# Kernel tuning notes

Hardware: AMD Instinct MI355X
Metric: run time of the kernel (lower is better)

Reference implementation:

```python
import jax, jax.numpy as jnp
import numpy as np

B, D, V = 1024, 512, 100000
M = 0.4
EPS = 1e-07


def setup_inputs() -> dict:
    key = jax.random.key(0)
    k1, k2, k3 = jax.random.split(key, 3)
    inp = jax.random.normal(k1, (B, D), dtype=jnp.float32)
    # xavier_uniform for (D, V): limit = sqrt(6/(D+V))
    limit = float(np.sqrt(6.0 / (D + V)))
    weight = jax.random.uniform(k2, (D, V), dtype=jnp.float32, minval=-limit, maxval=limit)
    labels = jax.random.randint(k3, (B,), 0, V, dtype=jnp.int64)
    return {"input": inp, "weight": weight, "labels": labels}


def reference(input, weight, labels):
    # L2-normalize rows of input and columns of weight (F.normalize eps=1e-12)
    x_norm = input / jnp.maximum(jnp.linalg.norm(input, axis=1, keepdims=True), 1e-12)
    w_norm = weight / jnp.maximum(jnp.linalg.norm(weight, axis=0, keepdims=True), 1e-12)
    cosine = x_norm @ w_norm                                # [B, V]
    cosine = jnp.clip(cosine, -1.0 + EPS, 1.0 - EPS)
    arcos = jnp.arccos(cosine)
    # add margin m only at the label class (one-hot add without dense one-hot)
    rows = jnp.arange(B)
    arcos = arcos.at[rows, labels].add(M)
    logits = jnp.cos(arcos)                                 # [B, V]
    # cross-entropy, mean reduction
    logz = jax.nn.logsumexp(logits, axis=1)                 # [B]
    label_logit = logits[rows, labels]                      # [B]
    loss = jnp.mean(logz - label_logit)
    return loss
```

## Files before the change

### kernel.cpp

```cpp
#include <hip/hip_runtime.h>
#include <hip/hip_bf16.h>
#include <math.h>

#define B_    1024
#define D_    512
#define V_    100000
#define V_PAD 100096
#define NT_   782
#define EPS_  1e-7f
#define COSM  0.9210609940028851f
#define SINM  0.3894183423086505f

typedef __bf16 bf16x8 __attribute__((ext_vector_type(8)));
typedef float  f32x4  __attribute__((ext_vector_type(4)));

struct alignas(16) US8 { unsigned short h[8]; };

__device__ __forceinline__ unsigned short f2bf(float f) {
  union { float f; unsigned u; } a; a.f = f;
  unsigned u = a.u;
  u += 0x7FFFu + ((u >> 16) & 1u);
  return (unsigned short)(u >> 16);
}

__device__ __forceinline__ void async_copy16(void* lds, const void* g) {
  __builtin_amdgcn_global_load_lds(
      (const __attribute__((address_space(1))) void*)g,
      (__attribute__((address_space(3))) void*)lds, 16, 0, 0);
}

__global__ void x_prep(const float* __restrict__ x,
                       unsigned short* __restrict__ xb,
                       float* __restrict__ S) {
  int t = threadIdx.x;
  int lane = t & 63, wave = t >> 6;
  int row = blockIdx.x * 4 + wave;
  const float* xr = x + (size_t)row * D_;
  f32x4 a = *(const f32x4*)(xr + lane * 8);
  f32x4 b = *(const f32x4*)(xr + lane * 8 + 4);
  float ss = a[0]*a[0] + a[1]*a[1] + a[2]*a[2] + a[3]*a[3]
           + b[0]*b[0] + b[1]*b[1] + b[2]*b[2] + b[3]*b[3];
#pragma unroll
  for (int off = 32; off > 0; off >>= 1) ss += __shfl_xor(ss, off, 64);
  float inv = 1.0f / fmaxf(sqrtf(ss), 1e-12f);
  US8 pk;
#pragma unroll
  for (int j = 0; j < 4; ++j) pk.h[j]     = f2bf(a[j] * inv);
#pragma unroll
  for (int j = 0; j < 4; ++j) pk.h[4 + j] = f2bf(b[j] * inv);
  *(US8*)(xb + (size_t)row * D_ + lane * 8) = pk;
  if (lane == 0) S[row] = 0.0f;
}

__global__ __launch_bounds__(256) void w_cast2(const float* __restrict__ w,
                                               unsigned short* __restrict__ wbT,
                                               float* __restrict__ invw) {
  __shared__ unsigned short tile[64 * 512];
  __shared__ float red[4][64];
  int t = threadIdx.x;
  int c = t & 63;
  int wv = t >> 6;
  int vb = blockIdx.x * 64;
  bool valid = (vb + c) < V_;
  const float* wp = w + vb + c;
  float ss = 0.0f;
#pragma unroll
  for (int k = 0; k < 16; ++k) {
    int d0 = k * 32 + wv * 8;
    float v[8];
#pragma unroll
    for (int i = 0; i < 8; ++i)
      v[i] = valid ? wp[(size_t)(d0 + i) * V_] : 0.0f;
    US8 pk;
#pragma unroll
    for (int i = 0; i < 8; ++i) { ss += v[i] * v[i]; pk.h[i] = f2bf(v[i]); }
    int chunk = ((d0 >> 3) ^ c) & 63;
    *(US8*)&tile[c * 512 + chunk * 8] = pk;
  }
  red[wv][c] = ss;
  __syncthreads();
  if (t < 64) {
    float tot = red[0][t] + red[1][t] + red[2][t] + red[3][t];
    invw[vb + t] = ((vb + t) < V_) ? 1.0f / fmaxf(sqrtf(tot), 1e-12f) : 0.0f;
  }
#pragma unroll
  for (int i = 0; i < 16; ++i) {
    int cc = wv * 16 + i;
    US8 val = *(const US8*)&tile[cc * 512 + ((c ^ cc) & 63) * 8];
    *(US8*)(wbT + (size_t)(vb + cc) * D_ + c * 8) = val;
  }
}

#define BM 128
#define BN 128
#define BK 64

__global__ __launch_bounds__(256) void gemm_epi(
    const unsigned short* __restrict__ xb,
    const unsigned short* __restrict__ wbT,
    const float* __restrict__ invw,
    const int* __restrict__ labels,
    float* __restrict__ S, float* __restrict__ Lb) {
  int bid = blockIdx.x;
  int xcd = bid & 7;
  int slot = bid >> 3;
  int tn = xcd * 98 + (slot >> 3);
  int tm = slot & 7;
  if (tn >= NT_) return;
  int m0 = tm * BM, n0 = tn * BN;

  __shared__ unsigned short Ab[BM * BK];
  __shared__ unsigned short Bb[BN * BK];
  __shared__ int labT[BM];
  int t = threadIdx.x;
  if (t < BM) labT[t] = labels[m0 + t];
  int lane = t & 63;
  int q = lane >> 4, l15 = lane & 15;
  int wave = t >> 6;
  int wm = (wave & 1) * 64, wn = (wave >> 1) * 64;
  f32x4 acc[4][4] = {};

  const unsigned short* gA[4];
  const unsigned short* gB[4];
#pragma unroll
  for (int j = 0; j < 4; ++j) {
    int p = t + 256 * j;
    int m = p >> 3;
    int kc = (p & 7) ^ (m & 7);
    gA[j] = xb  + (size_t)(m0 + m) * D_ + kc * 8;
    gB[j] = wbT + (size_t)(n0 + m) * D_ + kc * 8;
  }

  for (int kt = 0; kt < D_; kt += BK) {
#pragma unroll
    for (int j = 0; j < 4; ++j) {
      async_copy16(Ab + (t + 256 * j) * 8, gA[j] + kt);
      async_copy16(Bb + (t + 256 * j) * 8, gB[j] + kt);
    }
    __syncthreads();
    int h = l15 & 7;
#pragma unroll
    for (int s = 0; s < 2; ++s) {
      int kx = s * 4 + q;
      bf16x8 af[4], bfr[4];
#pragma unroll
      for (int ri = 0; ri < 4; ++ri) {
        int row = wm + ri * 16 + l15;
        af[ri] = *(const bf16x8*)&Ab[(row * 8 + (kx ^ h)) * 8];
      }
#pragma unroll
      for (int ci = 0; ci < 4; ++ci) {
        int row = wn + ci * 16 + l15;
        bfr[ci] = *(const bf16x8*)&Bb[(row * 8 + (kx ^ h)) * 8];
      }
#pragma unroll
      for (int ri = 0; ri < 4; ++ri)
#pragma unroll
        for (int ci = 0; ci < 4; ++ci)
          acc[ri][ci] = __builtin_amdgcn_mfma_f32_16x16x32_bf16(
              af[ri], bfr[ci], acc[ri][ci], 0, 0, 0);
    }
    __syncthreads();
  }

  float iw[4]; int vcol[4];
#pragma unroll
  for (int ci = 0; ci < 4; ++ci) {
    vcol[ci] = n0 + wn + ci * 16 + l15;
    iw[ci] = invw[vcol[ci]];
  }
#pragma unroll
  for (int ri = 0; ri < 4; ++ri) {
#pragma unroll
    for (int reg = 0; reg < 4; ++reg) {
      int ml = wm + ri * 16 + q * 4 + reg;
      int r = m0 + ml;
      int lab = labT[ml];
      float s = 0.0f;
#pragma unroll
      for (int ci = 0; ci < 4; ++ci) {
        float cv = acc[ri][ci][reg] * iw[ci];
        cv = fminf(fmaxf(cv, -1.0f + EPS_), 1.0f - EPS_);
        float logit = cv;
        if (vcol[ci] == lab) {
          logit = cv * COSM - sqrtf(fmaxf(1.0f - cv * cv, 0.0f)) * SINM;
          Lb[r] = logit;
        }
        s += (vcol[ci] < V_) ? __expf(logit) : 0.0f;
      }
      s += __shfl_xor(s, 1, 64);
      s += __shfl_xor(s, 2, 64);
      s += __shfl_xor(s, 4, 64);
      s += __shfl_xor(s, 8, 64);
      if (l15 == 0) atomicAdd(&S[r], s);
    }
  }
}

__global__ void finalk(const float* __restrict__ S, const float* __restrict__ Lb,
                       float* __restrict__ out) {
  __shared__ float red[256];
  int t = threadIdx.x;
  float s = 0.0f;
  for (int i = t; i < B_; i += 256) s += logf(S[i]) - Lb[i];
  red[t] = s;
  __syncthreads();
  for (int o = 128; o > 0; o >>= 1) {
    if (t < o) red[t] += red[t + o];
    __syncthreads();
  }
  if (t == 0) out[0] = red[0] * (1.0f / B_);
}

extern "C" void kernel_launch(void* const* d_in, const int* in_sizes, int n_in,
                              void* d_out, int out_size, void* d_ws, size_t ws_size,
                              hipStream_t stream) {
  const float* x = (const float*)d_in[0];
  const float* w = (const float*)d_in[1];
  const int* labels = (const int*)d_in[2];
  float* out = (float*)d_out;
  char* ws = (char*)d_ws;
  unsigned short* wbT = (unsigned short*)ws;
  unsigned short* xb  = (unsigned short*)(ws + 102498304ull);
  float* invw = (float*)(ws + 103546880ull);
  float* S    = (float*)(ws + 103947264ull);
  float* Lb   = (float*)(ws + 103951360ull);

  x_prep<<<256, 256, 0, stream>>>(x, xb, S);
  w_cast2<<<1564, 256, 0, stream>>>(w, wbT, invw);
  gemm_epi<<<6272, 256, 0, stream>>>(xb, wbT, invw, labels, S, Lb);
  finalk<<<1, 256, 0, stream>>>(S, Lb, out);
}
```

Measured before the change: 539.9 us.

## Fuse weight bf16 cast and column-norm computation into the GEMM main loop

Removes the separate w_cast2 pass that wrote a transposed bf16 copy of the weight plus inverse column norms. The GEMM now loads fp32 weight tiles directly, converts them to bf16 into swizzled LDS, and accumulates column sums of squares to build the inverse norms in the epilogue. This avoids a full write and reread of the 100 MB bf16 weight copy and one kernel launch. In exchange, each weight tile is read and converted by all 8 row-tile blocks. The fp32 loads are synchronous register loads rather than async LDS copies, which may expose memory latency in the K loop.

```diff
diff --git a/kernel.cpp b/kernel.cpp
--- a/kernel.cpp
+++ b/kernel.cpp
@@ -5,7 +5,6 @@
 #define B_    1024
 #define D_    512
 #define V_    100000
-#define V_PAD 100096
 #define NT_   782
 #define EPS_  1e-7f
 #define COSM  0.9210609940028851f
@@ -52,53 +51,13 @@
   if (lane == 0) S[row] = 0.0f;
 }
 
-__global__ __launch_bounds__(256) void w_cast2(const float* __restrict__ w,
-                                               unsigned short* __restrict__ wbT,
-                                               float* __restrict__ invw) {
-  __shared__ unsigned short tile[64 * 512];
-  __shared__ float red[4][64];
-  int t = threadIdx.x;
-  int c = t & 63;
-  int wv = t >> 6;
-  int vb = blockIdx.x * 64;
-  bool valid = (vb + c) < V_;
-  const float* wp = w + vb + c;
-  float ss = 0.0f;
-#pragma unroll
-  for (int k = 0; k < 16; ++k) {
-    int d0 = k * 32 + wv * 8;
-    float v[8];
-#pragma unroll
-    for (int i = 0; i < 8; ++i)
-      v[i] = valid ? wp[(size_t)(d0 + i) * V_] : 0.0f;
-    US8 pk;
-#pragma unroll
-    for (int i = 0; i < 8; ++i) { ss += v[i] * v[i]; pk.h[i] = f2bf(v[i]); }
-    int chunk = ((d0 >> 3) ^ c) & 63;
-    *(US8*)&tile[c * 512 + chunk * 8] = pk;
-  }
-  red[wv][c] = ss;
-  __syncthreads();
-  if (t < 64) {
-    float tot = red[0][t] + red[1][t] + red[2][t] + red[3][t];
-    invw[vb + t] = ((vb + t) < V_) ? 1.0f / fmaxf(sqrtf(tot), 1e-12f) : 0.0f;
-  }
-#pragma unroll
-  for (int i = 0; i < 16; ++i) {
-    int cc = wv * 16 + i;
-    US8 val = *(const US8*)&tile[cc * 512 + ((c ^ cc) & 63) * 8];
-    *(US8*)(wbT + (size_t)(vb + cc) * D_ + c * 8) = val;
-  }
-}
-
 #define BM 128
 #define BN 128
 #define BK 64
 
-__global__ __launch_bounds__(256) void gemm_epi(
+__global__ __launch_bounds__(256) void gemm_fused(
     const unsigned short* __restrict__ xb,
-    const unsigned short* __restrict__ wbT,
-    const float* __restrict__ invw,
+    const float* __restrict__ w,
     const int* __restrict__ labels,
     float* __restrict__ S, float* __restrict__ Lb) {
   int bid = blockIdx.x;
@@ -111,6 +70,8 @@
 
   __shared__ unsigned short Ab[BM * BK];
   __shared__ unsigned short Bb[BN * BK];
+  __shared__ float sqred[8][BN];
+  __shared__ float iwL[BN];
   __shared__ int labT[BM];
   int t = threadIdx.x;
   if (t < BM) labT[t] = labels[m0 + t];
@@ -121,22 +82,55 @@
   f32x4 acc[4][4] = {};
 
   const unsigned short* gA[4];
-  const unsigned short* gB[4];
+  unsigned short* lA[4];
 #pragma unroll
   for (int j = 0; j < 4; ++j) {
     int p = t + 256 * j;
     int m = p >> 3;
     int kc = (p & 7) ^ (m & 7);
-    gA[j] = xb  + (size_t)(m0 + m) * D_ + kc * 8;
-    gB[j] = wbT + (size_t)(n0 + m) * D_ + kc * 8;
-  }
+    gA[j] = xb + (size_t)(m0 + m) * D_ + kc * 8;
+    lA[j] = Ab + p * 8;
+  }
+
+  int cg = t & 31;
+  int rp = t >> 5;
+  int c0l = cg * 4;
+  bool vok = (n0 + c0l + 3) < V_;
+  const float* wbase = w + (size_t)rp * 8 * V_ + n0 + c0l;
+  unsigned short* bdst[4];
+#pragma unroll
+  for (int cc = 0; cc < 4; ++cc) {
+    int col = c0l + cc;
+    bdst[cc] = &Bb[(col * 8 + (rp ^ (col & 7))) * 8];
+  }
+  float ssq[4] = {0.0f, 0.0f, 0.0f, 0.0f};
 
   for (int kt = 0; kt < D_; kt += BK) {
 #pragma unroll
-    for (int j = 0; j < 4; ++j) {
-      async_copy16(Ab + (t + 256 * j) * 8, gA[j] + kt);
-      async_copy16(Bb + (t + 256 * j) * 8, gB[j] + kt);
-    }
+    for (int j = 0; j < 4; ++j) async_copy16(lA[j], gA[j] + kt);
+
+    f32x4 row[8];
+    if (vok) {
+#pragma unroll
+      for (int i = 0; i < 8; ++i)
+        row[i] = *(const f32x4*)(wbase + (size_t)i * V_);
+    } else {
+#pragma unroll
+      for (int i = 0; i < 8; ++i) row[i] = f32x4{0.0f, 0.0f, 0.0f, 0.0f};
+    }
+#pragma unroll
+    for (int cc = 0; cc < 4; ++cc) {
+      US8 pk;
+#pragma unroll
+      for (int i = 0; i < 8; ++i) {
+        float v = row[i][cc];
+        ssq[cc] += v * v;
+        pk.h[i] = f2bf(v);
+      }
+      *(US8*)bdst[cc] = pk;
+    }
+    wbase += (size_t)BK * V_;
+
     __syncthreads();
     int h = l15 & 7;
 #pragma unroll
@@ -145,13 +139,13 @@
       bf16x8 af[4], bfr[4];
 #pragma unroll
       for (int ri = 0; ri < 4; ++ri) {
-        int row = wm + ri * 16 + l15;
-        af[ri] = *(const bf16x8*)&Ab[(row * 8 + (kx ^ h)) * 8];
+        int row_ = wm + ri * 16 + l15;
+        af[ri] = *(const bf16x8*)&Ab[(row_ * 8 + (kx ^ h)) * 8];
       }
 #pragma unroll
       for (int ci = 0; ci < 4; ++ci) {
-        int row = wn + ci * 16 + l15;
-        bfr[ci] = *(const bf16x8*)&Bb[(row * 8 + (kx ^ h)) * 8];
+        int row_ = wn + ci * 16 + l15;
+        bfr[ci] = *(const bf16x8*)&Bb[(row_ * 8 + (kx ^ h)) * 8];
       }
 #pragma unroll
       for (int ri = 0; ri < 4; ++ri)
@@ -163,11 +157,23 @@
     __syncthreads();
   }
 
+#pragma unroll
+  for (int cc = 0; cc < 4; ++cc) sqred[rp][c0l + cc] = ssq[cc];
+  __syncthreads();
+  if (t < BN) {
+    float tot = 0.0f;
+#pragma unroll
+    for (int p = 0; p < 8; ++p) tot += sqred[p][t];
+    iwL[t] = ((n0 + t) < V_) ? 1.0f / fmaxf(sqrtf(tot), 1e-12f) : 0.0f;
+  }
+  __syncthreads();
+
   float iw[4]; int vcol[4];
 #pragma unroll
   for (int ci = 0; ci < 4; ++ci) {
-    vcol[ci] = n0 + wn + ci * 16 + l15;
-    iw[ci] = invw[vcol[ci]];
+    int nl = wn + ci * 16 + l15;
+    vcol[ci] = n0 + nl;
+    iw[ci] = iwL[nl];
   }
 #pragma unroll
   for (int ri = 0; ri < 4; ++ri) {
@@ -220,14 +226,11 @@
   const int* labels = (const int*)d_in[2];
   float* out = (float*)d_out;
   char* ws = (char*)d_ws;
-  unsigned short* wbT = (unsigned short*)ws;
-  unsigned short* xb  = (unsigned short*)(ws + 102498304ull);
-  float* invw = (float*)(ws + 103546880ull);
-  float* S    = (float*)(ws + 103947264ull);
-  float* Lb   = (float*)(ws + 103951360ull);
+  unsigned short* xb = (unsigned short*)ws;
+  float* S  = (float*)(ws + 1048576ull);
+  float* Lb = (float*)(ws + 1052672ull);
 
   x_prep<<<256, 256, 0, stream>>>(x, xb, S);
-  w_cast2<<<1564, 256, 0, stream>>>(w, wbT, invw);
-  gemm_epi<<<6272, 256, 0, stream>>>(xb, wbT, invw, labels, S, Lb);
+  gemm_fused<<<6272, 256, 0, stream>>>(xb, w, labels, S, Lb);
   finalk<<<1, 256, 0, stream>>>(S, Lb, out);
 }
```

Measured after the change: 517.3 us. 4.2% less time.
